# Performance work log

Hardware: AMD Instinct MI355X
Metric: run time of the kernel (lower is better)

The kernel has to match this reference:

```python
import jax, jax.numpy as jnp
import numpy as np
from jax import lax

B, C_IN, T = 64, 40, 8192

def conv1d(x, w, b):
    # x: [B,C,T], w: [O,I,K] (torch Conv1d layout), stride 2, VALID padding
    y = lax.conv_general_dilated(x, w, window_strides=(2,), padding='VALID',
                                 dimension_numbers=('NCH', 'OIH', 'NCH'))
    return y + b[None, :, None]

def avgpool2(x):
    # AvgPool1d(kernel=2, stride=2): pairwise mean, drop trailing odd element
    t2 = x.shape[-1] // 2
    return x[..., :2 * t2].reshape(x.shape[0], x.shape[1], t2, 2).mean(-1)

def setup_inputs():
    key = jax.random.key(0)
    ks = jax.random.split(key, 24)
    def w_init(k, shape, fan_in):
        return jax.random.normal(k, shape, jnp.float32) * (1.0 / np.sqrt(fan_in))
    inp = {}
    inp['x_input'] = jax.random.normal(ks[0], (B, C_IN, T), jnp.float32)
    # per-sample valid lengths in [2048, 8192] so the deep strided stack leaves >=1 frame
    inp['len_mask'] = 2048 + jax.random.randint(ks[1], (B,), 0, T - 2048 + 1, dtype=jnp.int32)
    convs = [(96, C_IN, 10), (96, 96, 5), (96, 96, 5), (96, 96, 5), (96, 96, 5), (96, 96, 5), (128, 96, 3)]
    for i, (o, ci, k) in enumerate(convs):
        inp[f'w{i+1}'] = w_init(ks[2 + 2 * i], (o, ci, k), ci * k)
        inp[f'b{i+1}'] = jnp.zeros((o,), jnp.float32)
    lins = [(128, 128), (64, 128), (5, 64)]
    for i, (o, ci) in enumerate(lins):
        inp[f'lw{i+1}'] = w_init(ks[16 + 2 * i], (o, ci), ci)
        inp[f'lb{i+1}'] = jnp.zeros((o,), jnp.float32)
    return inp

def reference(x_input, len_mask, w1, b1, w2, b2, w3, b3, w4, b4, w5, b5, w6, b6, w7, b7,
              lw1, lb1, lw2, lb2, lw3, lb3):
    # Batched masked equivalent of the per-sample ragged loop: for VALID stride-2 convs,
    # output position j depends only on inputs < valid length when j < valid out-length,
    # so we run batched convs on padded input and track per-sample valid lengths.
    Lv = len_mask.astype(jnp.int32)
    x = jax.nn.relu(conv1d(x_input, w1, b1)); Lv = (Lv - 10) // 2 + 1
    x = jax.nn.relu(conv1d(x, w2, b2));       Lv = (Lv - 5) // 2 + 1
    x = jax.nn.relu(conv1d(x, w3, b3));       Lv = (Lv - 5) // 2 + 1
    # cnn_1d_top (dropout in eval mode = identity)
    x = conv1d(x, w4, b4);        Lv = (Lv - 5) // 2 + 1
    x = jax.nn.relu(avgpool2(x)); Lv = Lv // 2
    x = conv1d(x, w5, b5);        Lv = (Lv - 5) // 2 + 1
    x = jax.nn.relu(avgpool2(x)); Lv = Lv // 2
    x = jax.nn.relu(conv1d(x, w6, b6)); Lv = (Lv - 5) // 2 + 1
    x = jax.nn.relu(conv1d(x, w7, b7)); Lv = (Lv - 3) // 2 + 1
    # AdaptiveMaxPool1d(1) over each sample's valid region
    mask = jnp.arange(x.shape[-1])[None, :] < Lv[:, None]          # [B, T_out]
    x = jnp.max(jnp.where(mask[:, None, :], x, -jnp.inf), axis=-1)  # [B, 128]
    # out1_top MLP head
    h = jax.nn.relu(x @ lw1.T + lb1)
    h = jax.nn.relu(h @ lw2.T + lb2)
    return h @ lw3.T + lb3
```

## Files before the change

### kernel.cpp

```cpp
#include <hip/hip_runtime.h>
#include <hip/hip_bf16.h>
#include <math.h>


typedef __attribute__((ext_vector_type(8))) _Float16 f16x8;
typedef __attribute__((ext_vector_type(4))) float f32x4;

__device__ __forceinline__ unsigned short f2h_bits(float f) {
    union { _Float16 h; unsigned short u; } cv;
    cv.h = (_Float16)f;
    return cv.u;
}

template<int KEFF, int CI, int NBLK, bool IN_FP32, bool RELU, bool OUT_F16, bool POOL>
__global__ __launch_bounds__(512, 4)
void conv_nb(const unsigned short* __restrict__ xh,
             const unsigned short* __restrict__ wpk,
             const float* __restrict__ bias,
             unsigned short* __restrict__ yh,
             float* __restrict__ yf,
             int Tin, int Tout)
{
    constexpr int CO    = 96;
    constexpr int NTHR  = 512;
    constexpr int GTOT  = CI * KEFF;
    constexpr int STEPS = (GTOT + 31) / 32;
    constexpr int RD    = NBLK + KEFF / 2;
    constexpr int NTW   = NBLK / 64;
    constexpr int TOT   = CI * RD;
    constexpr int NIT   = (TOT + NTHR - 1) / NTHR;

    __shared__ unsigned int Bs[TOT];

    const int tid  = threadIdx.x;
    const int lane = tid & 63;
    const int wave = tid >> 6;
    const int mg   = wave & 1;
    const int tg   = wave >> 1;
    const int quad = lane >> 4;
    const int l16  = lane & 15;
    const int wc0  = tg * (NBLK / 4);

    const int nT = (Tout + NBLK - 1) / NBLK;
    const int b  = blockIdx.x / nT;
    const int t0 = (blockIdx.x % nT) * NBLK;

    const float* xf = (const float*)xh;
    const unsigned int* xb = (const unsigned int*)xh + (((size_t)b * CI * Tin) >> 1);
    const int rowd = Tin >> 1;

    #pragma unroll
    for (int it = 0; it < NIT; ++it) {
        int i = tid + it * NTHR;
        if (i < TOT) {
            int r = (unsigned)i / (unsigned)RD, d = i - r * RD;
            unsigned int v;
            if (IN_FP32) {
                int e = 2 * (t0 + d);
                if (e > Tin - 2) e = Tin - 2;
                const float* src = xf + ((size_t)b * CI + r) * Tin + e;
                float2 w = *(const float2*)src;
                v = (unsigned int)f2h_bits(w.x) | ((unsigned int)f2h_bits(w.y) << 16);
            } else {
                v = *(xb + (size_t)r * rowd + t0 + d);
            }
            Bs[i] = v;
        }
    }
    __syncthreads();

    f32x4 acc[3][NTW];
    #pragma unroll
    for (int mt = 0; mt < 3; ++mt)
        #pragma unroll
        for (int nt = 0; nt < NTW; ++nt) acc[mt][nt] = (f32x4)0.f;

    #pragma unroll
    for (int s = 0; s < STEPS; ++s) {
        int offp[4];
        #pragma unroll
        for (int p = 0; p < 4; ++p) {
            int g = 32 * s + quad * 8 + 2 * p;
            if (g > GTOT - 2) g = GTOT - 2;
            unsigned ci = (unsigned)g / (unsigned)KEFF;
            unsigned dwo = ((unsigned)g - ci * (unsigned)KEFF) >> 1;
            offp[p] = (int)ci * RD + wc0 + l16 + (int)dwo;
        }

        union { unsigned int u[4]; f16x8 v; } Bv[NTW];
        #pragma unroll
        for (int nt = 0; nt < NTW; ++nt)
            #pragma unroll
            for (int p = 0; p < 4; ++p) Bv[nt].u[p] = Bs[offp[p] + nt * 16];

        const unsigned short* ap = wpk + (size_t)s * 6144 + (size_t)lane * 8;
        #pragma unroll
        for (int mt = 0; mt < 3; ++mt) {
            f16x8 Ah = *(const f16x8*)(ap + (mg * 3 + mt) * 512);
            f16x8 Al = *(const f16x8*)(ap + (6 + mg * 3 + mt) * 512);
            #pragma unroll
            for (int nt = 0; nt < NTW; ++nt)
                acc[mt][nt] = __builtin_amdgcn_mfma_f32_16x16x32_f16(Ah, Bv[nt].v, acc[mt][nt], 0, 0, 0);
            #pragma unroll
            for (int nt = 0; nt < NTW; ++nt)
                acc[mt][nt] = __builtin_amdgcn_mfma_f32_16x16x32_f16(Al, Bv[nt].v, acc[mt][nt], 0, 0, 0);
        }
    }

    #pragma unroll
    for (int mt = 0; mt < 3; ++mt) {
        #pragma unroll
        for (int r = 0; r < 4; ++r) {
            int o = (mg * 3 + mt) * 16 + quad * 4 + r;
            float bv = bias[o];
            #pragma unroll
            for (int nt = 0; nt < NTW; ++nt) {
                int t = t0 + wc0 + nt * 16 + l16;
                float v = acc[mt][nt][r] + bv;
                if (RELU) v = fmaxf(v, 0.f);
                if (POOL) {
                    float sum = v + __shfl_xor(v, 1, 64);
                    if ((lane & 1) == 0 && t + 1 < Tout) {
                        float pr = fmaxf(0.5f * sum, 0.f);
                        size_t pidx = ((size_t)b * CO + o) * (Tout >> 1) + (t >> 1);
                        if (OUT_F16) yh[pidx] = f2h_bits(pr);
                        else         yf[pidx] = pr;
                    }
                } else if (t < Tout) {
                    size_t oidx = ((size_t)b * CO + o) * Tout + t;
                    if (OUT_F16) yh[oidx] = f2h_bits(v);
                    else         yf[oidx] = v;
                }
            }
        }
    }
}

__device__ __forceinline__ void repack_img(const float* __restrict__ w,
                                           unsigned short* __restrict__ wpk,
                                           int idx, int KP, int KW, int CI)
{
    int j = idx & 7, lane = (idx >> 3) & 63, g = idx >> 9;
    int c = g / 24, r = g % 24;
    int mt = r % 6, sh = r / 6;
    int half = sh & 1, s = sh >> 1;
    int S  = c * 2 + s;
    int kg = S * 32 + (lane >> 4) * 8 + j;
    int o  = mt * 16 + (lane & 15);
    int ci = kg / KP, k = kg - ci * KP;
    float val = (ci < CI && k < KW) ? w[((size_t)o * CI + ci) * KW + k] : 0.f;
    _Float16 hh = (_Float16)val;
    union { _Float16 h; unsigned short u; } cv;
    cv.h = (half == 0) ? hh : (_Float16)(val - (float)hh);
    wpk[idx] = cv.u;
}
__device__ __forceinline__ void repack_okc(const float* __restrict__ w,
                                           float* __restrict__ wr,
                                           int idx, int CI, int K, int CO)
{
    int o = idx % CO; int rem = idx / CO; int k = rem % K; int ci = rem / K;
    wr[idx] = w[((size_t)o * CI + ci) * K + k];
}

__global__ void repack_all(const float* w1, const float* w2, const float* w3,
                           const float* w4, const float* w5, const float* w6,
                           const float* w7,
                           unsigned short* p1, unsigned short* p2,
                           unsigned short* p3, unsigned short* p4,
                           unsigned short* p5, float* r6, float* r7)
{
    int idx = blockIdx.x * 256 + threadIdx.x;
    if (idx < 79872)  { repack_img(w1, p1, idx, 10, 10, 40); return; }
    idx -= 79872;
    if (idx < 110592) { repack_img(w2, p2, idx, 6, 5, 96); return; }
    idx -= 110592;
    if (idx < 110592) { repack_img(w3, p3, idx, 6, 5, 96); return; }
    idx -= 110592;
    if (idx < 110592) { repack_img(w4, p4, idx, 6, 5, 96); return; }
    idx -= 110592;
    if (idx < 110592) { repack_img(w5, p5, idx, 6, 5, 96); return; }
    idx -= 110592;
    if (idx < 46080)  { repack_okc(w6, r6, idx, 96, 5, 96); return; }
    idx -= 46080;
    if (idx < 36864)  { repack_okc(w7, r7, idx, 96, 3, 128); return; }
}

__global__ __launch_bounds__(256)
void conv6_k(const float* __restrict__ y5p, const float* __restrict__ w6r,
             const float* __restrict__ b6, float* __restrict__ y6)
{
    __shared__ float s5[96 * 62];
    const int b = blockIdx.x >> 2, ob = blockIdx.x & 3;
    const int tid = threadIdx.x;
    for (int i = tid; i < 96 * 62; i += 256) s5[i] = y5p[(size_t)b * 96 * 62 + i];
    __syncthreads();

    const int wave = __builtin_amdgcn_readfirstlane(tid >> 6);
    const int t = tid & 63;
    if (t < 29) {
        const int o0 = ob * 24 + wave * 6;
        float a[6];
        #pragma unroll
        for (int oo = 0; oo < 6; oo++) a[oo] = 0.f;
        for (int ci = 0; ci < 96; ci++) {
            float xr[5];
            #pragma unroll
            for (int k = 0; k < 5; k++) xr[k] = s5[ci * 62 + 2 * t + k];
            #pragma unroll
            for (int k = 0; k < 5; k++) {
                const float* wp = w6r + (ci * 5 + k) * 96 + o0;
                #pragma unroll
                for (int oo = 0; oo < 6; oo++)
                    a[oo] = fmaf(wp[oo], xr[k], a[oo]);
            }
        }
        #pragma unroll
        for (int oo = 0; oo < 6; oo++)
            y6[((size_t)b * 96 + o0 + oo) * 29 + t] = fmaxf(a[oo] + b6[o0 + oo], 0.f);
    }
}

__global__ __launch_bounds__(256)
void tail2(const float* __restrict__ y6,
           const float* __restrict__ w7r, const float* __restrict__ b7,
           const int* __restrict__ lens,
           const float* __restrict__ lw1, const float* __restrict__ lb1,
           const float* __restrict__ lw2, const float* __restrict__ lb2,
           const float* __restrict__ lw3, const float* __restrict__ lb3,
           float* __restrict__ out)
{
    __shared__ float s6[96 * 29 + 8];
    __shared__ float s7[128 * 14];
    __shared__ float feat[128], h1[128], h2[64];

    const int b = blockIdx.x, tid = threadIdx.x;
    for (int i = tid; i < 96 * 29; i += 256) s6[i] = y6[(size_t)b * 96 * 29 + i];
    __syncthreads();

    const int wave = __builtin_amdgcn_readfirstlane(tid >> 6);
    const int lane = tid & 63;
    const int sub  = lane >> 4;
    const int tl   = lane & 15;
    {
        float a[32];
        #pragma unroll
        for (int oo = 0; oo < 32; oo++) a[oo] = 0.f;
        const int ci0 = sub * 24;
        for (int ci = ci0; ci < ci0 + 24; ci++) {
            float xr[3];
            #pragma unroll
            for (int k = 0; k < 3; k++) xr[k] = s6[ci * 29 + 2 * tl + k];
            #pragma unroll
            for (int k = 0; k < 3; k++) {
                const float* wp = w7r + (ci * 3 + k) * 128 + wave * 32;
                #pragma unroll
                for (int oo = 0; oo < 32; oo++)
                    a[oo] = fmaf(wp[oo], xr[k], a[oo]);
            }
        }
        #pragma unroll
        for (int oo = 0; oo < 32; oo++) {
            float v = a[oo];
            v += __shfl_xor(v, 16, 64);
            v += __shfl_xor(v, 32, 64);
            if (sub == 0 && tl < 14) {
                int o = wave * 32 + oo;
                s7[o * 14 + tl] = fmaxf(v + b7[o], 0.f);
            }
        }
    }
    __syncthreads();

    if (tid < 128) {
        int L = lens[b];
        L = (L - 10) / 2 + 1;
        L = (L - 5) / 2 + 1;
        L = (L - 5) / 2 + 1;
        L = (L - 5) / 2 + 1;
        L = L / 2;
        L = (L - 5) / 2 + 1;
        L = L / 2;
        L = (L - 5) / 2 + 1;
        L = (L - 3) / 2 + 1;
        float m = -INFINITY;
        for (int t = 0; t < L; t++) m = fmaxf(m, s7[tid * 14 + t]);
        feat[tid] = m;
    }
    __syncthreads();

    if (tid < 128) {
        float s = lb1[tid];
        for (int i = 0; i < 128; i++) s = fmaf(lw1[tid * 128 + i], feat[i], s);
        h1[tid] = fmaxf(s, 0.f);
    }
    __syncthreads();
    if (tid < 64) {
        float s = lb2[tid];
        for (int i = 0; i < 128; i++) s = fmaf(lw2[tid * 128 + i], h1[i], s);
        h2[tid] = fmaxf(s, 0.f);
    }
    __syncthreads();
    if (tid < 5) {
        float s = lb3[tid];
        for (int i = 0; i < 64; i++) s = fmaf(lw3[tid * 64 + i], h2[i], s);
        out[b * 5 + tid] = s;
    }
}

extern "C" void kernel_launch(void* const* d_in, const int* in_sizes, int n_in,
                              void* d_out, int out_size, void* d_ws, size_t ws_size,
                              hipStream_t stream)
{
    const float* x    = (const float*)d_in[0];
    const int*   lens = (const int*)  d_in[1];
    const float* w1 = (const float*)d_in[2];   const float* b1 = (const float*)d_in[3];
    const float* w2 = (const float*)d_in[4];   const float* b2 = (const float*)d_in[5];
    const float* w3 = (const float*)d_in[6];   const float* b3 = (const float*)d_in[7];
    const float* w4 = (const float*)d_in[8];   const float* b4 = (const float*)d_in[9];
    const float* w5 = (const float*)d_in[10];  const float* b5 = (const float*)d_in[11];
    const float* w6 = (const float*)d_in[12];  const float* b6 = (const float*)d_in[13];
    const float* w7 = (const float*)d_in[14];  const float* b7 = (const float*)d_in[15];
    const float* lw1 = (const float*)d_in[16]; const float* lb1 = (const float*)d_in[17];
    const float* lw2 = (const float*)d_in[18]; const float* lb2 = (const float*)d_in[19];
    const float* lw3 = (const float*)d_in[20]; const float* lb3 = (const float*)d_in[21];
    float* out = (float*)d_out;
    char*  W   = (char*)d_ws;

    size_t off = 0;
    auto take = [&](size_t bytes) {
        size_t o = off; off = (off + bytes + 255) & ~(size_t)255; return o;
    };
    size_t o_y3h = take(((size_t)64 * 96 * 1020 + 2048) * 2);
    size_t o_y4h = take(((size_t)64 * 96 * 254 + 2048) * 2);
    size_t o_y5p = take((size_t)64 * 96 * 62 * 4 + 1024);
    size_t o_y6  = take((size_t)64 * 96 * 29 * 4);
    size_t o_wp1 = take((size_t)79872 * 2);
    size_t o_wp2 = take((size_t)110592 * 2);
    size_t o_wp3 = take((size_t)110592 * 2);
    size_t o_wp4 = take((size_t)110592 * 2);
    size_t o_wp5 = take((size_t)110592 * 2);
    size_t o_w6r = take((size_t)46080 * 4);
    size_t o_w7r = take((size_t)36864 * 4);
    size_t persist = off;

    auto chunk_bytes = [&](int Bc) -> size_t {
        size_t s = 0;
        s += ((size_t)Bc * 96 * 4092 + 2048) * 2 + 256;
        s += ((size_t)Bc * 96 * 2044 + 2048) * 2 + 256;
        return s;
    };
    int Bc = 64;
    while (Bc > 1 && persist + chunk_bytes(Bc) > ws_size) Bc >>= 1;
    size_t o_y1h = take(((size_t)Bc * 96 * 4092 + 2048) * 2);
    size_t o_y2h = take(((size_t)Bc * 96 * 2044 + 2048) * 2);

    auto US = [&](size_t o) { return (unsigned short*)(W + o); };
    auto FP = [&](size_t o) { return (float*)(W + o); };

    repack_all<<<dim3((605184 + 255) / 256), 256, 0, stream>>>(
        w1, w2, w3, w4, w5, w6, w7,
        US(o_wp1), US(o_wp2), US(o_wp3), US(o_wp4), US(o_wp5),
        FP(o_w6r), FP(o_w7r));

    const int nchunks = 64 / Bc;
    for (int c = 0; c < nchunks; c++) {
        const float* xc = x + (size_t)c * Bc * 40 * 8192;

        conv_nb<10, 40, 256, true, true, true, false><<<dim3(Bc * 16), 512, 0, stream>>>(
            (const unsigned short*)xc, US(o_wp1), b1, US(o_y1h), nullptr, 8192, 4092);
        conv_nb< 6, 96, 128, false, true, true, false><<<dim3(Bc * 16), 512, 0, stream>>>(
            US(o_y1h), US(o_wp2), b2, US(o_y2h), nullptr, 4092, 2044);
        unsigned short* y3h_c = US(o_y3h) + (size_t)c * Bc * 96 * 1020;
        conv_nb< 6, 96, 128, false, true, true, false><<<dim3(Bc * 8), 512, 0, stream>>>(
            US(o_y2h), US(o_wp3), b3, y3h_c, nullptr, 2044, 1020);
    }

    conv_nb<6, 96, 128, false, false, true, true><<<dim3(64 * 4), 512, 0, stream>>>(
        US(o_y3h), US(o_wp4), b4, US(o_y4h), nullptr, 1020, 508);

    conv_nb<6, 96, 64, false, false, false, true><<<dim3(64 * 2), 512, 0, stream>>>(
        US(o_y4h), US(o_wp5), b5, nullptr, FP(o_y5p), 254, 125);

    conv6_k<<<dim3(256), 256, 0, stream>>>(FP(o_y5p), FP(o_w6r), b6, FP(o_y6));

    tail2<<<dim3(64), 256, 0, stream>>>(
        FP(o_y6), FP(o_w7r), b7, lens, lw1, lb1, lw2, lb2, lw3, lb3, out);
}
```

Baseline: 403.2 us.

## Double-buffer MFMA operand fragments and shrink conv1/conv4 time tiles

Restructures the conv_nb inner loop so the A (weight) and B (LDS activation) fragments for the next K-step are loaded into a second register set while the current step's MFMAs run. The aim is to hide global and LDS load latency behind matrix ops. Separately, conv1 and conv4 use half the time-tile width with twice as many blocks, giving more parallelism across CUs. Double buffering raises register pressure under launch_bounds(512,4), and smaller tiles re-stage more halo input.

```diff
diff --git a/kernel.cpp b/kernel.cpp
--- a/kernel.cpp
+++ b/kernel.cpp
@@ -75,8 +75,9 @@
         #pragma unroll
         for (int nt = 0; nt < NTW; ++nt) acc[mt][nt] = (f32x4)0.f;
 
-    #pragma unroll
-    for (int s = 0; s < STEPS; ++s) {
+    union BvU { unsigned int u[4]; f16x8 v; };
+
+    auto loadBfrag = [&](int s, BvU (&Bv)[NTW]) {
         int offp[4];
         #pragma unroll
         for (int p = 0; p < 4; ++p) {
@@ -86,25 +87,43 @@
             unsigned dwo = ((unsigned)g - ci * (unsigned)KEFF) >> 1;
             offp[p] = (int)ci * RD + wc0 + l16 + (int)dwo;
         }
-
-        union { unsigned int u[4]; f16x8 v; } Bv[NTW];
         #pragma unroll
         for (int nt = 0; nt < NTW; ++nt)
             #pragma unroll
             for (int p = 0; p < 4; ++p) Bv[nt].u[p] = Bs[offp[p] + nt * 16];
-
-        const unsigned short* ap = wpk + (size_t)s * 6144 + (size_t)lane * 8;
+    };
+    auto loadAfrag = [&](int s, f16x8 (&Ah)[3], f16x8 (&Al)[3]) {
+        const unsigned short* ap = wpk + (size_t)s * 6144 + (size_t)lane * 8
+                                 + (size_t)mg * 1536;
         #pragma unroll
         for (int mt = 0; mt < 3; ++mt) {
-            f16x8 Ah = *(const f16x8*)(ap + (mg * 3 + mt) * 512);
-            f16x8 Al = *(const f16x8*)(ap + (6 + mg * 3 + mt) * 512);
+            Ah[mt] = *(const f16x8*)(ap + mt * 512);
+            Al[mt] = *(const f16x8*)(ap + 3072 + mt * 512);
+        }
+    };
+    auto mfma_step = [&](BvU (&Bv)[NTW], f16x8 (&Ah)[3], f16x8 (&Al)[3]) {
+        #pragma unroll
+        for (int mt = 0; mt < 3; ++mt)
             #pragma unroll
             for (int nt = 0; nt < NTW; ++nt)
-                acc[mt][nt] = __builtin_amdgcn_mfma_f32_16x16x32_f16(Ah, Bv[nt].v, acc[mt][nt], 0, 0, 0);
+                acc[mt][nt] = __builtin_amdgcn_mfma_f32_16x16x32_f16(Ah[mt], Bv[nt].v, acc[mt][nt], 0, 0, 0);
+        #pragma unroll
+        for (int mt = 0; mt < 3; ++mt)
             #pragma unroll
             for (int nt = 0; nt < NTW; ++nt)
-                acc[mt][nt] = __builtin_amdgcn_mfma_f32_16x16x32_f16(Al, Bv[nt].v, acc[mt][nt], 0, 0, 0);
-        }
+                acc[mt][nt] = __builtin_amdgcn_mfma_f32_16x16x32_f16(Al[mt], Bv[nt].v, acc[mt][nt], 0, 0, 0);
+    };
+
+    BvU  BvA[NTW], BvB[NTW];
+    f16x8 AhA[3], AlA[3], AhB[3], AlB[3];
+
+    loadBfrag(0, BvA); loadAfrag(0, AhA, AlA);
+    #pragma unroll
+    for (int ss = 0; ss < STEPS; ss += 2) {
+        if (ss + 1 < STEPS) { loadBfrag(ss + 1, BvB); loadAfrag(ss + 1, AhB, AlB); }
+        mfma_step(BvA, AhA, AlA);
+        if (ss + 2 < STEPS) { loadBfrag(ss + 2, BvA); loadAfrag(ss + 2, AhA, AlA); }
+        if (ss + 1 < STEPS) mfma_step(BvB, AhB, AlB);
     }
 
     #pragma unroll
@@ -366,7 +385,7 @@
     for (int c = 0; c < nchunks; c++) {
         const float* xc = x + (size_t)c * Bc * 40 * 8192;
 
-        conv_nb<10, 40, 256, true, true, true, false><<<dim3(Bc * 16), 512, 0, stream>>>(
+        conv_nb<10, 40, 128, true, true, true, false><<<dim3(Bc * 32), 512, 0, stream>>>(
             (const unsigned short*)xc, US(o_wp1), b1, US(o_y1h), nullptr, 8192, 4092);
         conv_nb< 6, 96, 128, false, true, true, false><<<dim3(Bc * 16), 512, 0, stream>>>(
             US(o_y1h), US(o_wp2), b2, US(o_y2h), nullptr, 4092, 2044);
@@ -375,7 +394,7 @@
             US(o_y2h), US(o_wp3), b3, y3h_c, nullptr, 2044, 1020);
     }
 
-    conv_nb<6, 96, 128, false, false, true, true><<<dim3(64 * 4), 512, 0, stream>>>(
+    conv_nb<6, 96, 64, false, false, true, true><<<dim3(64 * 8), 512, 0, stream>>>(
         US(o_y3h), US(o_wp4), b4, US(o_y4h), nullptr, 1020, 508);
 
     conv_nb<6, 96, 64, false, false, false, true><<<dim3(64 * 2), 512, 0, stream>>>(
```

Result: no change. 396.7 us (-1.6%).

## Pad K=5 conv taps to 8 for precomputed LDS offsets and batched weight loads

Applied to the files above, without the earlier changes.

For the K=5 stride-2 convs, the padded effective tap count goes from 6 to 8, so each 32-wide reduction step covers whole input channels. LDS gather offsets can then be computed once per thread and reused with a constant stride instead of doing per-step integer division. Weight fragments for a step are loaded together before the MFMAs, occupancy hints drop from 4 to 2 blocks per CU, and conv4 switches to a smaller time tile with more blocks. In exchange, the padding adds about a third more MFMA work and more packed-weight traffic for these layers.

```diff
diff --git a/kernel.cpp b/kernel.cpp
--- a/kernel.cpp
+++ b/kernel.cpp
@@ -13,7 +13,7 @@
 }
 
 template<int KEFF, int CI, int NBLK, bool IN_FP32, bool RELU, bool OUT_F16, bool POOL>
-__global__ __launch_bounds__(512, 4)
+__global__ __launch_bounds__(512, 2)
 void conv_nb(const unsigned short* __restrict__ xh,
              const unsigned short* __restrict__ wpk,
              const float* __restrict__ bias,
@@ -29,6 +29,8 @@
     constexpr int NTW   = NBLK / 64;
     constexpr int TOT   = CI * RD;
     constexpr int NIT   = (TOT + NTHR - 1) / NTHR;
+    constexpr int PH    = (32 % KEFF == 0) ? 1 : 5;
+    constexpr int PERRD = (32 * PH / KEFF) * RD;
 
     __shared__ unsigned int Bs[TOT];
 
@@ -62,12 +64,25 @@
                 float2 w = *(const float2*)src;
                 v = (unsigned int)f2h_bits(w.x) | ((unsigned int)f2h_bits(w.y) << 16);
             } else {
-                v = *(xb + (size_t)r * rowd + t0 + d);
+                int dd = t0 + d;
+                if (dd > rowd - 1) dd = rowd - 1;
+                v = *(xb + (size_t)r * rowd + dd);
             }
             Bs[i] = v;
         }
     }
     __syncthreads();
+
+    int offb[PH][4];
+    #pragma unroll
+    for (int ph = 0; ph < PH; ++ph)
+        #pragma unroll
+        for (int p = 0; p < 4; ++p) {
+            int g = 32 * ph + quad * 8 + 2 * p;
+            unsigned ci = (unsigned)g / (unsigned)KEFF;
+            unsigned dwo = ((unsigned)g - ci * (unsigned)KEFF) >> 1;
+            offb[ph][p] = (int)ci * RD + wc0 + l16 + (int)dwo;
+        }
 
     f32x4 acc[3][NTW];
     #pragma unroll
@@ -77,34 +92,44 @@
 
     #pragma unroll
     for (int s = 0; s < STEPS; ++s) {
-        int offp[4];
-        #pragma unroll
-        for (int p = 0; p < 4; ++p) {
-            int g = 32 * s + quad * 8 + 2 * p;
-            if (g > GTOT - 2) g = GTOT - 2;
-            unsigned ci = (unsigned)g / (unsigned)KEFF;
-            unsigned dwo = ((unsigned)g - ci * (unsigned)KEFF) >> 1;
-            offp[p] = (int)ci * RD + wc0 + l16 + (int)dwo;
-        }
-
-        union { unsigned int u[4]; f16x8 v; } Bv[NTW];
-        #pragma unroll
-        for (int nt = 0; nt < NTW; ++nt)
-            #pragma unroll
-            for (int p = 0; p < 4; ++p) Bv[nt].u[p] = Bs[offp[p] + nt * 16];
-
-        const unsigned short* ap = wpk + (size_t)s * 6144 + (size_t)lane * 8;
+        union BvU { unsigned int u[4]; f16x8 v; } Bv[NTW];
+        if (32 * (s + 1) <= GTOT) {
+            #pragma unroll
+            for (int nt = 0; nt < NTW; ++nt)
+                #pragma unroll
+                for (int p = 0; p < 4; ++p)
+                    Bv[nt].u[p] = Bs[offb[s % PH][p] + (s / PH) * PERRD + nt * 16];
+        } else {
+            #pragma unroll
+            for (int nt = 0; nt < NTW; ++nt)
+                #pragma unroll
+                for (int p = 0; p < 4; ++p) {
+                    int g = 32 * s + quad * 8 + 2 * p;
+                    if (g > GTOT - 2) g = GTOT - 2;
+                    unsigned ci = (unsigned)g / (unsigned)KEFF;
+                    unsigned dwo = ((unsigned)g - ci * (unsigned)KEFF) >> 1;
+                    Bv[nt].u[p] = Bs[(int)ci * RD + wc0 + l16 + (int)dwo + nt * 16];
+                }
+        }
+
+        const unsigned short* ap = wpk + (size_t)s * 6144 + (size_t)(mg * 3) * 512
+                                 + (size_t)lane * 8;
+        f16x8 Ah[3], Al[3];
         #pragma unroll
         for (int mt = 0; mt < 3; ++mt) {
-            f16x8 Ah = *(const f16x8*)(ap + (mg * 3 + mt) * 512);
-            f16x8 Al = *(const f16x8*)(ap + (6 + mg * 3 + mt) * 512);
+            Ah[mt] = *(const f16x8*)(ap + mt * 512);
+            Al[mt] = *(const f16x8*)(ap + 3072 + mt * 512);
+        }
+        #pragma unroll
+        for (int mt = 0; mt < 3; ++mt)
             #pragma unroll
             for (int nt = 0; nt < NTW; ++nt)
-                acc[mt][nt] = __builtin_amdgcn_mfma_f32_16x16x32_f16(Ah, Bv[nt].v, acc[mt][nt], 0, 0, 0);
+                acc[mt][nt] = __builtin_amdgcn_mfma_f32_16x16x32_f16(Ah[mt], Bv[nt].v, acc[mt][nt], 0, 0, 0);
+        #pragma unroll
+        for (int mt = 0; mt < 3; ++mt)
             #pragma unroll
             for (int nt = 0; nt < NTW; ++nt)
-                acc[mt][nt] = __builtin_amdgcn_mfma_f32_16x16x32_f16(Al, Bv[nt].v, acc[mt][nt], 0, 0, 0);
-        }
+                acc[mt][nt] = __builtin_amdgcn_mfma_f32_16x16x32_f16(Al[mt], Bv[nt].v, acc[mt][nt], 0, 0, 0);
     }
 
     #pragma unroll
@@ -172,14 +197,14 @@
     int idx = blockIdx.x * 256 + threadIdx.x;
     if (idx < 79872)  { repack_img(w1, p1, idx, 10, 10, 40); return; }
     idx -= 79872;
-    if (idx < 110592) { repack_img(w2, p2, idx, 6, 5, 96); return; }
-    idx -= 110592;
-    if (idx < 110592) { repack_img(w3, p3, idx, 6, 5, 96); return; }
-    idx -= 110592;
-    if (idx < 110592) { repack_img(w4, p4, idx, 6, 5, 96); return; }
-    idx -= 110592;
-    if (idx < 110592) { repack_img(w5, p5, idx, 6, 5, 96); return; }
-    idx -= 110592;
+    if (idx < 147456) { repack_img(w2, p2, idx, 8, 5, 96); return; }
+    idx -= 147456;
+    if (idx < 147456) { repack_img(w3, p3, idx, 8, 5, 96); return; }
+    idx -= 147456;
+    if (idx < 147456) { repack_img(w4, p4, idx, 8, 5, 96); return; }
+    idx -= 147456;
+    if (idx < 147456) { repack_img(w5, p5, idx, 8, 5, 96); return; }
+    idx -= 147456;
     if (idx < 46080)  { repack_okc(w6, r6, idx, 96, 5, 96); return; }
     idx -= 46080;
     if (idx < 36864)  { repack_okc(w7, r7, idx, 96, 3, 128); return; }
@@ -335,10 +360,10 @@
     size_t o_y5p = take((size_t)64 * 96 * 62 * 4 + 1024);
     size_t o_y6  = take((size_t)64 * 96 * 29 * 4);
     size_t o_wp1 = take((size_t)79872 * 2);
-    size_t o_wp2 = take((size_t)110592 * 2);
-    size_t o_wp3 = take((size_t)110592 * 2);
-    size_t o_wp4 = take((size_t)110592 * 2);
-    size_t o_wp5 = take((size_t)110592 * 2);
+    size_t o_wp2 = take((size_t)147456 * 2);
+    size_t o_wp3 = take((size_t)147456 * 2);
+    size_t o_wp4 = take((size_t)147456 * 2);
+    size_t o_wp5 = take((size_t)147456 * 2);
     size_t o_w6r = take((size_t)46080 * 4);
     size_t o_w7r = take((size_t)36864 * 4);
     size_t persist = off;
@@ -357,7 +382,7 @@
     auto US = [&](size_t o) { return (unsigned short*)(W + o); };
     auto FP = [&](size_t o) { return (float*)(W + o); };
 
-    repack_all<<<dim3((605184 + 255) / 256), 256, 0, stream>>>(
+    repack_all<<<dim3((752640 + 255) / 256), 256, 0, stream>>>(
         w1, w2, w3, w4, w5, w6, w7,
         US(o_wp1), US(o_wp2), US(o_wp3), US(o_wp4), US(o_wp5),
         FP(o_w6r), FP(o_w7r));
@@ -368,17 +393,17 @@
 
         conv_nb<10, 40, 256, true, true, true, false><<<dim3(Bc * 16), 512, 0, stream>>>(
             (const unsigned short*)xc, US(o_wp1), b1, US(o_y1h), nullptr, 8192, 4092);
-        conv_nb< 6, 96, 128, false, true, true, false><<<dim3(Bc * 16), 512, 0, stream>>>(
+        conv_nb< 8, 96, 128, false, true, true, false><<<dim3(Bc * 16), 512, 0, stream>>>(
             US(o_y1h), US(o_wp2), b2, US(o_y2h), nullptr, 4092, 2044);
         unsigned short* y3h_c = US(o_y3h) + (size_t)c * Bc * 96 * 1020;
-        conv_nb< 6, 96, 128, false, true, true, false><<<dim3(Bc * 8), 512, 0, stream>>>(
+        conv_nb< 8, 96, 128, false, true, true, false><<<dim3(Bc * 8), 512, 0, stream>>>(
             US(o_y2h), US(o_wp3), b3, y3h_c, nullptr, 2044, 1020);
     }
 
-    conv_nb<6, 96, 128, false, false, true, true><<<dim3(64 * 4), 512, 0, stream>>>(
+    conv_nb<8, 96, 64, false, false, true, true><<<dim3(64 * 8), 512, 0, stream>>>(
         US(o_y3h), US(o_wp4), b4, US(o_y4h), nullptr, 1020, 508);
 
-    conv_nb<6, 96, 64, false, false, false, true><<<dim3(64 * 2), 512, 0, stream>>>(
+    conv_nb<8, 96, 64, false, false, false, true><<<dim3(64 * 2), 512, 0, stream>>>(
         US(o_y4h), US(o_wp5), b5, nullptr, FP(o_y5p), 254, 125);
 
     conv6_k<<<dim3(256), 256, 0, stream>>>(FP(o_y5p), FP(o_w6r), b6, FP(o_y6));
```

Measured after the change: 414.1 us. +2.7%, slower.
